# Kernel optimization log

Hardware: AMD Instinct MI355X
Metric: run time of the kernel (lower is better)

## Reference

```python
import jax, jax.numpy as jnp
import numpy as np

B, N, D, H, CD = 2, 2048, 1024, 16, 3
HD = D // H


def setup_inputs() -> dict:
    key = jax.random.key(0)
    ks = jax.random.split(key, 6)
    x = jax.random.normal(ks[0], (B, N, D), dtype=jnp.float32)
    coords = jax.random.normal(ks[1], (B, N, CD), dtype=jnp.float32)
    attn_bias = jax.random.normal(ks[2], (N, N), dtype=jnp.float32) * 0.1
    Wqkv = jax.random.normal(ks[3], (D, 3 * D), dtype=jnp.float32) * (1.0 / np.sqrt(D))
    bqkv = jnp.zeros((3 * D,), dtype=jnp.float32)
    rel_weight = jax.random.normal(ks[4], (H, CD), dtype=jnp.float32) * 0.02
    return {"x": x, "coords": coords, "attn_bias": attn_bias, "Wqkv": Wqkv,
            "bqkv": bqkv, "rel_weight": rel_weight}


def reference(x, coords, attn_bias, Wqkv, bqkv, rel_weight):
    b, n, d = x.shape
    h, hd = H, HD
    qkv = x @ Wqkv + bqkv                       # (B,N,3D)
    q, k, v = jnp.split(qkv, 3, axis=-1)
    # reshape_for_mha: (B,N,D) -> (B,H,N,hd)
    def heads(t):
        return t.reshape(b, n, h, hd).transpose(0, 2, 1, 3)
    qh, kh, vh = heads(q), heads(k), heads(v)
    # coord_proj[b,h,n] = coords[b,n,:] @ rel_weight[h,:]
    coord_proj = jnp.einsum('bnc,hc->bhn', coords.astype(jnp.float32), rel_weight)
    # flex_attention: scale by 1/sqrt(head_dim) BEFORE score_mod
    scores = jnp.einsum('bhqd,bhkd->bhqk', qh, kh) / np.sqrt(hd)
    scores = scores + coord_proj[:, :, :, None] - coord_proj[:, :, None, :]
    scores = scores + attn_bias[None, None, :, :]   # '2d' additive mask bias
    attn = jax.nn.softmax(scores, axis=-1)
    yh = jnp.einsum('bhqk,bhkd->bhqd', attn, vh)    # (B,H,N,hd)
    return yh.transpose(0, 2, 1, 3).reshape(b, n, d)
```

## Files before the change

kernel.cpp:

```cpp
#include <hip/hip_runtime.h>
#include <hip/hip_bf16.h>
#include <math.h>

typedef __hip_bfloat16 bf16;
typedef __bf16  bf16x8 __attribute__((ext_vector_type(8)));
typedef float   f32x4  __attribute__((ext_vector_type(4)));

#define BB 2
#define NN 2048
#define DD 1024
#define HH 16
#define HD 64
#define LOG2E   1.44269504f
#define SCALE_Q 0.18033688f

__device__ __forceinline__ void glds16(const bf16* g, bf16* l) {
    __builtin_amdgcn_global_load_lds((const __attribute__((address_space(1))) void*)g,
                                     (__attribute__((address_space(3))) void*)l, 16, 0, 0);
}
__device__ __forceinline__ unsigned short bfu(float x) {
    bf16 b = __float2bfloat16(x);
    return __builtin_bit_cast(unsigned short, b);
}

__global__ __launch_bounds__(256) void prep(const float* __restrict__ x,
                                            const float* __restrict__ bias,
                                            const float* __restrict__ W,
                                            const float* __restrict__ coords,
                                            const float* __restrict__ relw,
                                            bf16* __restrict__ xb,
                                            float* __restrict__ pbf,
                                            bf16* __restrict__ Wt,
                                            bf16* __restrict__ cpn) {
    __shared__ bf16 tsm[64][65];
    const int bid = blockIdx.x, tid = threadIdx.x;
    if (bid < 2048) {
        size_t i = ((size_t)bid * 256 + tid) * 8;
        float4 a = *(const float4*)(x + i);
        float4 b = *(const float4*)(x + i + 4);
        bf16 t[8];
        t[0] = __float2bfloat16(a.x); t[1] = __float2bfloat16(a.y);
        t[2] = __float2bfloat16(a.z); t[3] = __float2bfloat16(a.w);
        t[4] = __float2bfloat16(b.x); t[5] = __float2bfloat16(b.y);
        t[6] = __float2bfloat16(b.z); t[7] = __float2bfloat16(b.w);
        *(int4*)(xb + i) = *(int4*)t;
    } else if (bid < 2560) {
        int t    = (bid - 2048) * 256 + tid;
        int lane = t & 63;
        int wave = (t >> 6) & 3;
        int kt   = (t >> 8) & 31;
        int Qb   = t >> 13;
        int quad = lane >> 4, l15 = lane & 15;
        float v[32];
#pragma unroll
        for (int j = 0; j < 32; ++j) {
            int qb = j >> 4, g = (j >> 2) & 3, r = j & 3;
            int q = Qb * 128 + wave * 32 + qb * 16 + quad * 4 + r;
            int k = kt * 64 + g * 16 + l15;
            v[j] = LOG2E * bias[(size_t)q * NN + k];
        }
        int4* dst = (int4*)(pbf + (size_t)t * 32);
#pragma unroll
        for (int i = 0; i < 8; ++i) dst[i] = ((int4*)v)[i];
    } else if (bid < 3328) {
        int idx = bid - 2560;
        int n0 = (idx % 48) * 64;
        int k0 = (idx / 48) * 64;
        int tx = tid & 63, tg = tid >> 6;
#pragma unroll
        for (int i = 0; i < 16; ++i) {
            int r = tg + i * 4;
            tsm[r][tx] = __float2bfloat16(W[(size_t)(k0 + r) * 3072 + n0 + tx]);
        }
        __syncthreads();
#pragma unroll
        for (int i = 0; i < 16; ++i) {
            int r = tg + i * 4;
            Wt[(size_t)(n0 + r) * 1024 + k0 + tx] = tsm[tx][r];
        }
    } else {
        int idx = (bid - 3328) * 256 + tid;
        int n  = idx & (NN - 1);
        int bh = idx >> 11;
        int h  = bh & (HH - 1);
        int b  = bh >> 4;
        float acc = 0.f;
#pragma unroll
        for (int c = 0; c < 3; ++c)
            acc += coords[(size_t)(b * NN + n) * 3 + c] * relw[h * 3 + c];
        cpn[idx] = __float2bfloat16(-LOG2E * acc);
    }
}

__global__ __launch_bounds__(256) void qkv_gemm(const bf16* __restrict__ X,
                                                const bf16* __restrict__ W,
                                                const float* __restrict__ bq,
                                                bf16* __restrict__ qo,
                                                bf16* __restrict__ ko,
                                                bf16* __restrict__ vo) {
    __shared__ __align__(16) bf16 As[128 * 32];
    __shared__ __align__(16) bf16 Bs[128 * 32];
    const int tid  = threadIdx.x;
    const int n0   = blockIdx.x * 128;
    const int m0   = blockIdx.y * 128;
    const int wave = tid >> 6, lane = tid & 63, l15 = lane & 15, quad = lane >> 4;
    const int wm   = wave >> 1, wn = wave & 1;

    f32x4 acc[4][4];
    const f32x4 z4 = {0.f, 0.f, 0.f, 0.f};
#pragma unroll
    for (int i = 0; i < 4; ++i)
#pragma unroll
        for (int j = 0; j < 4; ++j) acc[i][j] = z4;

    for (int kt = 0; kt < 1024; kt += 32) {
        __syncthreads();
#pragma unroll
        for (int j = 0; j < 2; ++j) {
            int s   = (wave * 2 + j) * 64 + lane;
            int row = s >> 2;
            int c   = (s & 3) ^ ((row >> 1) & 3);
            glds16(X + (size_t)(m0 + row) * 1024 + kt + c * 8, As + (wave * 2 + j) * 512);
            glds16(W + (size_t)(n0 + row) * 1024 + kt + c * 8, Bs + (wave * 2 + j) * 512);
        }
        __syncthreads();

        bf16x8 a[4], b[4];
#pragma unroll
        for (int mt = 0; mt < 4; ++mt) {
            int ra = wm * 64 + mt * 16 + l15;
            a[mt] = *(const bf16x8*)&As[ra * 32 + ((quad ^ ((ra >> 1) & 3)) * 8)];
        }
#pragma unroll
        for (int nt = 0; nt < 4; ++nt) {
            int rb = wn * 64 + nt * 16 + l15;
            b[nt] = *(const bf16x8*)&Bs[rb * 32 + ((quad ^ ((rb >> 1) & 3)) * 8)];
        }
#pragma unroll
        for (int mt = 0; mt < 4; ++mt)
#pragma unroll
            for (int nt = 0; nt < 4; ++nt)
                acc[mt][nt] = __builtin_amdgcn_mfma_f32_16x16x32_bf16(a[mt], b[nt], acc[mt][nt], 0, 0, 0);
    }

#pragma unroll
    for (int nt = 0; nt < 4; ++nt) {
        int c    = n0 + wn * 64 + nt * 16 + l15;
        int tsel = c >> 10;
        int rem  = c & 1023;
        int h    = rem >> 6, d = rem & 63;
        float bias = bq[c];
        float qs   = (tsel == 0) ? SCALE_Q : 1.0f;
        bf16* outp = (tsel == 0) ? qo : ((tsel == 1) ? ko : vo);
#pragma unroll
        for (int mt = 0; mt < 4; ++mt)
#pragma unroll
            for (int r = 0; r < 4; ++r) {
                int m = m0 + wm * 64 + mt * 16 + quad * 4 + r;
                int b = m >> 11, n = m & (NN - 1);
                outp[((size_t)(b * HH + h) * NN + n) * HD + d] =
                    __float2bfloat16((acc[mt][nt][r] + bias) * qs);
            }
    }
}

__global__ __launch_bounds__(256) void transpose_v(const bf16* __restrict__ vw,
                                                   bf16* __restrict__ vt) {
    __shared__ bf16 t[64][65];
    const int bh = blockIdx.y;
    const int n0 = blockIdx.x * 64;
    const size_t base = (size_t)bh * NN * HD;
    const int tx = threadIdx.x & 63, tg = threadIdx.x >> 6;
#pragma unroll
    for (int i = 0; i < 16; ++i) {
        int r = tg + i * 4;
        t[r][tx] = vw[base + (size_t)(n0 + r) * HD + tx];
    }
    __syncthreads();
#pragma unroll
    for (int i = 0; i < 16; ++i) {
        int d = tg + i * 4;
        vt[base + (size_t)d * NN + n0 + tx] = t[tx][d];
    }
}

__global__ __launch_bounds__(256, 3) void attn(const bf16* __restrict__ Q,
                                               const bf16* __restrict__ K,
                                               const bf16* __restrict__ Vt_g,
                                               const bf16* __restrict__ cpn_g,
                                               const float* __restrict__ pbf,
                                               float* __restrict__ out) {
    __shared__ __align__(16) bf16 Ks[2][64 * 64];
    __shared__ __align__(16) bf16 Vs[2][64 * 64];
    __shared__ __align__(16) unsigned PsW[4][16 * 36];
    __shared__ __align__(16) bf16 cpl[NN];
    const int tid  = threadIdx.x;
    const int Qb   = blockIdx.x;
    const int bh   = blockIdx.y;
    const int b    = bh >> 4, h = bh & 15;
    const int q0   = Qb * 128;
    const int wave = tid >> 6, lane = tid & 63, l15 = lane & 15, quad = lane >> 4;
    const size_t base = (size_t)bh * NN * HD;

    glds16(cpn_g + bh * NN + (wave * 64 + lane) * 8, cpl + wave * 512);

    bf16x8 qf0[2], qf1[2];
#pragma unroll
    for (int qb = 0; qb < 2; ++qb) {
        int qrow = q0 + wave * 32 + qb * 16 + l15;
        qf0[qb] = *(const bf16x8*)&Q[base + (size_t)qrow * HD + quad * 8];
        qf1[qb] = *(const bf16x8*)&Q[base + (size_t)qrow * HD + 32 + quad * 8];
    }

#pragma unroll
    for (int j = 0; j < 2; ++j) {
        int ss  = (wave * 2 + j) * 64 + lane;
        int row = ss >> 3;
        int c   = (ss & 7) ^ (row & 7);
        glds16(K    + base + (size_t)row * HD + c * 8,  Ks[0] + (wave * 2 + j) * 512);
        glds16(Vt_g + base + (size_t)row * NN + c * 8,  Vs[0] + (wave * 2 + j) * 512);
    }

    const f32x4 z4 = {0.f, 0.f, 0.f, 0.f};
    float l_loc[2][4];
    f32x4 o[2][4];
#pragma unroll
    for (int qb = 0; qb < 2; ++qb) {
#pragma unroll
        for (int r = 0; r < 4; ++r) l_loc[qb][r] = 0.f;
#pragma unroll
        for (int t = 0; t < 4; ++t) o[qb][t] = z4;
    }

    for (int t = 0; t < 32; ++t) {
        const int cur = t & 1;
        __syncthreads();
        if (t < 31) {
            int kk1 = (t + 1) * 64;
#pragma unroll
            for (int j = 0; j < 2; ++j) {
                int ss  = (wave * 2 + j) * 64 + lane;
                int row = ss >> 3;
                int c   = (ss & 7) ^ (row & 7);
                glds16(K    + base + (size_t)(kk1 + row) * HD + c * 8, Ks[cur ^ 1] + (wave * 2 + j) * 512);
                glds16(Vt_g + base + (size_t)row * NN + kk1 + c * 8,   Vs[cur ^ 1] + (wave * 2 + j) * 512);
            }
        }

        bf16x8 k0[4], k1[4];
#pragma unroll
        for (int g = 0; g < 4; ++g) {
            int krow = g * 16 + l15, sw = krow & 7;
            k0[g] = *(const bf16x8*)&Ks[cur][krow * 64 + ((quad ^ sw) * 8)];
            k1[g] = *(const bf16x8*)&Ks[cur][krow * 64 + (((4 + quad) ^ sw) * 8)];
        }

        f32x4 s[2][4];
#pragma unroll
        for (int qb = 0; qb < 2; ++qb)
#pragma unroll
            for (int g = 0; g < 4; ++g) {
                s[qb][g] = __builtin_amdgcn_mfma_f32_16x16x32_bf16(qf0[qb], k0[g], z4, 0, 0, 0);
                s[qb][g] = __builtin_amdgcn_mfma_f32_16x16x32_bf16(qf1[qb], k1[g], s[qb][g], 0, 0, 0);
            }

        float mg[4];
#pragma unroll
        for (int g = 0; g < 4; ++g)
            mg[g] = __bfloat162float(cpl[t * 64 + g * 16 + l15]);

        bf16x8 v0[4], v1[4];
#pragma unroll
        for (int tt = 0; tt < 4; ++tt) {
            int drow = tt * 16 + l15, sw = drow & 7;
            v0[tt] = *(const bf16x8*)&Vs[cur][drow * 64 + ((quad ^ sw) * 8)];
            v1[tt] = *(const bf16x8*)&Vs[cur][drow * 64 + (((4 + quad) ^ sw) * 8)];
        }

        const float* bsrc = pbf + ((((size_t)Qb * 32 + t) * 4 + wave) * 64 + lane) * 32;

#pragma unroll
        for (int qb = 0; qb < 2; ++qb) {
            float4 bv[4];
#pragma unroll
            for (int i = 0; i < 4; ++i) bv[i] = ((const float4*)(bsrc + qb * 16))[i];
            const float* bf = (const float*)bv;

            float p[4][4];
#pragma unroll
            for (int g = 0; g < 4; ++g)
#pragma unroll
                for (int r = 0; r < 4; ++r) {
                    float e = __builtin_amdgcn_exp2f(s[qb][g][r] + bf[g * 4 + r] + mg[g]);
                    p[g][r] = e;
                    l_loc[qb][r] += e;
                }
#pragma unroll
            for (int g2 = 0; g2 < 2; ++g2)
#pragma unroll
                for (int r = 0; r < 4; ++r) {
                    unsigned pk = (unsigned)bfu(p[g2][r]) | ((unsigned)bfu(p[g2 + 2][r]) << 16);
                    PsW[wave][(quad * 4 + r) * 36 + g2 * 16 + l15] = pk;
                }
            asm volatile("s_waitcnt lgkmcnt(0)" ::: "memory");
            const int4* pr = (const int4*)&PsW[wave][l15 * 36 + quad * 8];
            int4 da = pr[0], db = pr[1];
            union { unsigned u[4]; bf16x8 v; } u0, u1;
            u0.u[0] = __builtin_amdgcn_perm(da.y, da.x, 0x05040100u);
            u0.u[1] = __builtin_amdgcn_perm(da.w, da.z, 0x05040100u);
            u0.u[2] = __builtin_amdgcn_perm(db.y, db.x, 0x05040100u);
            u0.u[3] = __builtin_amdgcn_perm(db.w, db.z, 0x05040100u);
            u1.u[0] = __builtin_amdgcn_perm(da.y, da.x, 0x07060302u);
            u1.u[1] = __builtin_amdgcn_perm(da.w, da.z, 0x07060302u);
            u1.u[2] = __builtin_amdgcn_perm(db.y, db.x, 0x07060302u);
            u1.u[3] = __builtin_amdgcn_perm(db.w, db.z, 0x07060302u);
#pragma unroll
            for (int tt = 0; tt < 4; ++tt) {
                o[qb][tt] = __builtin_amdgcn_mfma_f32_16x16x32_bf16(u0.v, v0[tt], o[qb][tt], 0, 0, 0);
                o[qb][tt] = __builtin_amdgcn_mfma_f32_16x16x32_bf16(u1.v, v1[tt], o[qb][tt], 0, 0, 0);
            }
        }
    }

#pragma unroll
    for (int qb = 0; qb < 2; ++qb)
#pragma unroll
        for (int r = 0; r < 4; ++r) {
#pragma unroll
            for (int d = 1; d < 16; d <<= 1)
                l_loc[qb][r] += __shfl_xor(l_loc[qb][r], d, 64);
            float inv = 1.0f / l_loc[qb][r];
            int qq = q0 + wave * 32 + qb * 16 + quad * 4 + r;
#pragma unroll
            for (int tt = 0; tt < 4; ++tt)
                out[((size_t)(b * NN + qq)) * DD + h * HD + tt * 16 + l15] =
                    o[qb][tt][r] * inv;
        }
}

extern "C" void kernel_launch(void* const* d_in, const int* in_sizes, int n_in,
                              void* d_out, int out_size, void* d_ws, size_t ws_size,
                              hipStream_t stream) {
    const float* x      = (const float*)d_in[0];
    const float* coords = (const float*)d_in[1];
    const float* abias  = (const float*)d_in[2];
    const float* Wqkv   = (const float*)d_in[3];
    const float* bqkv   = (const float*)d_in[4];
    const float* relw   = (const float*)d_in[5];
    float* out = (float*)d_out;

    char* ws = (char*)d_ws;
    bf16*  xb  = (bf16*)(ws);
    bf16*  vt  = (bf16*)(ws);
    bf16*  qw  = (bf16*)(ws + 8388608);
    bf16*  kw  = (bf16*)(ws + 16777216);
    bf16*  vw  = (bf16*)(ws + 25165824);
    bf16*  Wt  = (bf16*)(ws + 33554432);
    float* pbf = (float*)(ws + 39845888);
    bf16*  cpb = (bf16*)(ws + 56623104);

    prep       <<<dim3(3584),   256, 0, stream>>>(x, abias, Wqkv, coords, relw,
                                                  xb, pbf, Wt, cpb);
    qkv_gemm   <<<dim3(24, 32), 256, 0, stream>>>(xb, Wt, bqkv, qw, kw, vw);
    transpose_v<<<dim3(32, 32), 256, 0, stream>>>(vw, vt);
    attn       <<<dim3(16, 32), 256, 0, stream>>>(qw, kw, vt, cpb, pbf, out);
}
```

Baseline: 233.9 us.

## Use 8-wave attention blocks and write V transposed directly from QKV GEMM

The attention kernel now runs 512 threads per block, with each wave handling 16 query rows instead of 32. This lowers per-wave register use and raises occupancy, and the prep kernel's precomputed bias layout is rearranged to match. The separate transpose_v kernel is dropped, and the QKV GEMM epilogue writes V straight into the head-dim-major layout. That saves a launch and a round trip through memory, at the cost of strided, uncoalesced scalar stores for V.

```diff
diff --git a/kernel.cpp b/kernel.cpp
--- a/kernel.cpp
+++ b/kernel.cpp
@@ -44,26 +44,26 @@
         t[4] = __float2bfloat16(b.x); t[5] = __float2bfloat16(b.y);
         t[6] = __float2bfloat16(b.z); t[7] = __float2bfloat16(b.w);
         *(int4*)(xb + i) = *(int4*)t;
-    } else if (bid < 2560) {
+    } else if (bid < 3072) {
         int t    = (bid - 2048) * 256 + tid;
         int lane = t & 63;
-        int wave = (t >> 6) & 3;
-        int kt   = (t >> 8) & 31;
-        int Qb   = t >> 13;
+        int wave = (t >> 6) & 7;
+        int kt   = (t >> 9) & 31;
+        int Qb   = t >> 14;
         int quad = lane >> 4, l15 = lane & 15;
-        float v[32];
-#pragma unroll
-        for (int j = 0; j < 32; ++j) {
-            int qb = j >> 4, g = (j >> 2) & 3, r = j & 3;
-            int q = Qb * 128 + wave * 32 + qb * 16 + quad * 4 + r;
+        float v[16];
+#pragma unroll
+        for (int j = 0; j < 16; ++j) {
+            int g = j >> 2, r = j & 3;
+            int q = Qb * 128 + wave * 16 + quad * 4 + r;
             int k = kt * 64 + g * 16 + l15;
             v[j] = LOG2E * bias[(size_t)q * NN + k];
         }
-        int4* dst = (int4*)(pbf + (size_t)t * 32);
-#pragma unroll
-        for (int i = 0; i < 8; ++i) dst[i] = ((int4*)v)[i];
-    } else if (bid < 3328) {
-        int idx = bid - 2560;
+        int4* dst = (int4*)(pbf + (size_t)t * 16);
+#pragma unroll
+        for (int i = 0; i < 4; ++i) dst[i] = ((int4*)v)[i];
+    } else if (bid < 3840) {
+        int idx = bid - 3072;
         int n0 = (idx % 48) * 64;
         int k0 = (idx / 48) * 64;
         int tx = tid & 63, tg = tid >> 6;
@@ -79,7 +79,7 @@
             Wt[(size_t)(n0 + r) * 1024 + k0 + tx] = tsm[tx][r];
         }
     } else {
-        int idx = (bid - 3328) * 256 + tid;
+        int idx = (bid - 3840) * 256 + tid;
         int n  = idx & (NN - 1);
         int bh = idx >> 11;
         int h  = bh & (HH - 1);
@@ -97,7 +97,7 @@
                                                 const float* __restrict__ bq,
                                                 bf16* __restrict__ qo,
                                                 bf16* __restrict__ ko,
-                                                bf16* __restrict__ vo) {
+                                                bf16* __restrict__ vt) {
     __shared__ __align__(16) bf16 As[128 * 32];
     __shared__ __align__(16) bf16 Bs[128 * 32];
     const int tid  = threadIdx.x;
@@ -151,40 +151,22 @@
         int h    = rem >> 6, d = rem & 63;
         float bias = bq[c];
         float qs   = (tsel == 0) ? SCALE_Q : 1.0f;
-        bf16* outp = (tsel == 0) ? qo : ((tsel == 1) ? ko : vo);
 #pragma unroll
         for (int mt = 0; mt < 4; ++mt)
 #pragma unroll
             for (int r = 0; r < 4; ++r) {
                 int m = m0 + wm * 64 + mt * 16 + quad * 4 + r;
                 int b = m >> 11, n = m & (NN - 1);
-                outp[((size_t)(b * HH + h) * NN + n) * HD + d] =
-                    __float2bfloat16((acc[mt][nt][r] + bias) * qs);
+                bf16 val = __float2bfloat16((acc[mt][nt][r] + bias) * qs);
+                if (tsel == 2)
+                    vt[((size_t)(b * HH + h) * HD + d) * NN + n] = val;
+                else
+                    ((tsel == 1) ? ko : qo)[((size_t)(b * HH + h) * NN + n) * HD + d] = val;
             }
     }
 }
 
-__global__ __launch_bounds__(256) void transpose_v(const bf16* __restrict__ vw,
-                                                   bf16* __restrict__ vt) {
-    __shared__ bf16 t[64][65];
-    const int bh = blockIdx.y;
-    const int n0 = blockIdx.x * 64;
-    const size_t base = (size_t)bh * NN * HD;
-    const int tx = threadIdx.x & 63, tg = threadIdx.x >> 6;
-#pragma unroll
-    for (int i = 0; i < 16; ++i) {
-        int r = tg + i * 4;
-        t[r][tx] = vw[base + (size_t)(n0 + r) * HD + tx];
-    }
-    __syncthreads();
-#pragma unroll
-    for (int i = 0; i < 16; ++i) {
-        int d = tg + i * 4;
-        vt[base + (size_t)d * NN + n0 + tx] = t[tx][d];
-    }
-}
-
-__global__ __launch_bounds__(256, 3) void attn(const bf16* __restrict__ Q,
+__global__ __launch_bounds__(512, 4) void attn(const bf16* __restrict__ Q,
                                                const bf16* __restrict__ K,
                                                const bf16* __restrict__ Vt_g,
                                                const bf16* __restrict__ cpn_g,
@@ -192,7 +174,7 @@
                                                float* __restrict__ out) {
     __shared__ __align__(16) bf16 Ks[2][64 * 64];
     __shared__ __align__(16) bf16 Vs[2][64 * 64];
-    __shared__ __align__(16) unsigned PsW[4][16 * 36];
+    __shared__ __align__(16) unsigned PsW[8][16 * 36];
     __shared__ __align__(16) bf16 cpl[NN];
     const int tid  = threadIdx.x;
     const int Qb   = blockIdx.x;
@@ -202,140 +184,113 @@
     const int wave = tid >> 6, lane = tid & 63, l15 = lane & 15, quad = lane >> 4;
     const size_t base = (size_t)bh * NN * HD;
 
-    glds16(cpn_g + bh * NN + (wave * 64 + lane) * 8, cpl + wave * 512);
-
-    bf16x8 qf0[2], qf1[2];
-#pragma unroll
-    for (int qb = 0; qb < 2; ++qb) {
-        int qrow = q0 + wave * 32 + qb * 16 + l15;
-        qf0[qb] = *(const bf16x8*)&Q[base + (size_t)qrow * HD + quad * 8];
-        qf1[qb] = *(const bf16x8*)&Q[base + (size_t)qrow * HD + 32 + quad * 8];
-    }
-
-#pragma unroll
-    for (int j = 0; j < 2; ++j) {
-        int ss  = (wave * 2 + j) * 64 + lane;
-        int row = ss >> 3;
-        int c   = (ss & 7) ^ (row & 7);
-        glds16(K    + base + (size_t)row * HD + c * 8,  Ks[0] + (wave * 2 + j) * 512);
-        glds16(Vt_g + base + (size_t)row * NN + c * 8,  Vs[0] + (wave * 2 + j) * 512);
+    if (wave < 4)
+        glds16(cpn_g + bh * NN + (wave * 64 + lane) * 8, cpl + wave * 512);
+
+    const int qrow = q0 + wave * 16 + l15;
+    bf16x8 qf0 = *(const bf16x8*)&Q[base + (size_t)qrow * HD + quad * 8];
+    bf16x8 qf1 = *(const bf16x8*)&Q[base + (size_t)qrow * HD + 32 + quad * 8];
+
+    {
+        int s   = wave * 64 + lane;
+        int row = s >> 3;
+        int c   = (s & 7) ^ (row & 7);
+        glds16(K    + base + (size_t)row * HD + c * 8, Ks[0] + wave * 512);
+        glds16(Vt_g + base + (size_t)row * NN + c * 8, Vs[0] + wave * 512);
     }
 
     const f32x4 z4 = {0.f, 0.f, 0.f, 0.f};
-    float l_loc[2][4];
-    f32x4 o[2][4];
-#pragma unroll
-    for (int qb = 0; qb < 2; ++qb) {
-#pragma unroll
-        for (int r = 0; r < 4; ++r) l_loc[qb][r] = 0.f;
-#pragma unroll
-        for (int t = 0; t < 4; ++t) o[qb][t] = z4;
-    }
+    float l_loc[4] = {0.f, 0.f, 0.f, 0.f};
+    f32x4 o[4];
+#pragma unroll
+    for (int t = 0; t < 4; ++t) o[t] = z4;
 
     for (int t = 0; t < 32; ++t) {
         const int cur = t & 1;
         __syncthreads();
         if (t < 31) {
             int kk1 = (t + 1) * 64;
-#pragma unroll
-            for (int j = 0; j < 2; ++j) {
-                int ss  = (wave * 2 + j) * 64 + lane;
-                int row = ss >> 3;
-                int c   = (ss & 7) ^ (row & 7);
-                glds16(K    + base + (size_t)(kk1 + row) * HD + c * 8, Ks[cur ^ 1] + (wave * 2 + j) * 512);
-                glds16(Vt_g + base + (size_t)row * NN + kk1 + c * 8,   Vs[cur ^ 1] + (wave * 2 + j) * 512);
-            }
-        }
-
-        bf16x8 k0[4], k1[4];
+            int s   = wave * 64 + lane;
+            int row = s >> 3;
+            int c   = (s & 7) ^ (row & 7);
+            glds16(K    + base + (size_t)(kk1 + row) * HD + c * 8, Ks[cur ^ 1] + wave * 512);
+            glds16(Vt_g + base + (size_t)row * NN + kk1 + c * 8,   Vs[cur ^ 1] + wave * 512);
+        }
+
+        f32x4 s4[4];
 #pragma unroll
         for (int g = 0; g < 4; ++g) {
             int krow = g * 16 + l15, sw = krow & 7;
-            k0[g] = *(const bf16x8*)&Ks[cur][krow * 64 + ((quad ^ sw) * 8)];
-            k1[g] = *(const bf16x8*)&Ks[cur][krow * 64 + (((4 + quad) ^ sw) * 8)];
-        }
-
-        f32x4 s[2][4];
-#pragma unroll
-        for (int qb = 0; qb < 2; ++qb)
-#pragma unroll
-            for (int g = 0; g < 4; ++g) {
-                s[qb][g] = __builtin_amdgcn_mfma_f32_16x16x32_bf16(qf0[qb], k0[g], z4, 0, 0, 0);
-                s[qb][g] = __builtin_amdgcn_mfma_f32_16x16x32_bf16(qf1[qb], k1[g], s[qb][g], 0, 0, 0);
-            }
-
+            bf16x8 k0 = *(const bf16x8*)&Ks[cur][krow * 64 + ((quad ^ sw) * 8)];
+            bf16x8 k1 = *(const bf16x8*)&Ks[cur][krow * 64 + (((4 + quad) ^ sw) * 8)];
+            s4[g] = __builtin_amdgcn_mfma_f32_16x16x32_bf16(qf0, k0, z4, 0, 0, 0);
+            s4[g] = __builtin_amdgcn_mfma_f32_16x16x32_bf16(qf1, k1, s4[g], 0, 0, 0);
+        }
+
+        float4 bv[4];
+        {
+            const float* bsrc = pbf + ((((size_t)Qb * 32 + t) * 8 + wave) * 64 + lane) * 16;
+#pragma unroll
+            for (int i = 0; i < 4; ++i) bv[i] = ((const float4*)bsrc)[i];
+        }
+        const float* bf = (const float*)bv;
         float mg[4];
 #pragma unroll
         for (int g = 0; g < 4; ++g)
             mg[g] = __bfloat162float(cpl[t * 64 + g * 16 + l15]);
 
-        bf16x8 v0[4], v1[4];
+        float p[4][4];
+#pragma unroll
+        for (int g = 0; g < 4; ++g)
+#pragma unroll
+            for (int r = 0; r < 4; ++r) {
+                float e = __builtin_amdgcn_exp2f(s4[g][r] + bf[g * 4 + r] + mg[g]);
+                p[g][r] = e;
+                l_loc[r] += e;
+            }
+
+#pragma unroll
+        for (int g2 = 0; g2 < 2; ++g2)
+#pragma unroll
+            for (int r = 0; r < 4; ++r) {
+                unsigned pk = (unsigned)bfu(p[g2][r]) | ((unsigned)bfu(p[g2 + 2][r]) << 16);
+                PsW[wave][(quad * 4 + r) * 36 + g2 * 16 + l15] = pk;
+            }
+        asm volatile("s_waitcnt lgkmcnt(0)" ::: "memory");
+        const int4* pr = (const int4*)&PsW[wave][l15 * 36 + quad * 8];
+        int4 da = pr[0], db = pr[1];
+        union { unsigned u[4]; bf16x8 v; } u0, u1;
+        u0.u[0] = __builtin_amdgcn_perm(da.y, da.x, 0x05040100u);
+        u0.u[1] = __builtin_amdgcn_perm(da.w, da.z, 0x05040100u);
+        u0.u[2] = __builtin_amdgcn_perm(db.y, db.x, 0x05040100u);
+        u0.u[3] = __builtin_amdgcn_perm(db.w, db.z, 0x05040100u);
+        u1.u[0] = __builtin_amdgcn_perm(da.y, da.x, 0x07060302u);
+        u1.u[1] = __builtin_amdgcn_perm(da.w, da.z, 0x07060302u);
+        u1.u[2] = __builtin_amdgcn_perm(db.y, db.x, 0x07060302u);
+        u1.u[3] = __builtin_amdgcn_perm(db.w, db.z, 0x07060302u);
+
 #pragma unroll
         for (int tt = 0; tt < 4; ++tt) {
             int drow = tt * 16 + l15, sw = drow & 7;
-            v0[tt] = *(const bf16x8*)&Vs[cur][drow * 64 + ((quad ^ sw) * 8)];
-            v1[tt] = *(const bf16x8*)&Vs[cur][drow * 64 + (((4 + quad) ^ sw) * 8)];
-        }
-
-        const float* bsrc = pbf + ((((size_t)Qb * 32 + t) * 4 + wave) * 64 + lane) * 32;
-
-#pragma unroll
-        for (int qb = 0; qb < 2; ++qb) {
-            float4 bv[4];
-#pragma unroll
-            for (int i = 0; i < 4; ++i) bv[i] = ((const float4*)(bsrc + qb * 16))[i];
-            const float* bf = (const float*)bv;
-
-            float p[4][4];
-#pragma unroll
-            for (int g = 0; g < 4; ++g)
-#pragma unroll
-                for (int r = 0; r < 4; ++r) {
-                    float e = __builtin_amdgcn_exp2f(s[qb][g][r] + bf[g * 4 + r] + mg[g]);
-                    p[g][r] = e;
-                    l_loc[qb][r] += e;
-                }
-#pragma unroll
-            for (int g2 = 0; g2 < 2; ++g2)
-#pragma unroll
-                for (int r = 0; r < 4; ++r) {
-                    unsigned pk = (unsigned)bfu(p[g2][r]) | ((unsigned)bfu(p[g2 + 2][r]) << 16);
-                    PsW[wave][(quad * 4 + r) * 36 + g2 * 16 + l15] = pk;
-                }
-            asm volatile("s_waitcnt lgkmcnt(0)" ::: "memory");
-            const int4* pr = (const int4*)&PsW[wave][l15 * 36 + quad * 8];
-            int4 da = pr[0], db = pr[1];
-            union { unsigned u[4]; bf16x8 v; } u0, u1;
-            u0.u[0] = __builtin_amdgcn_perm(da.y, da.x, 0x05040100u);
-            u0.u[1] = __builtin_amdgcn_perm(da.w, da.z, 0x05040100u);
-            u0.u[2] = __builtin_amdgcn_perm(db.y, db.x, 0x05040100u);
-            u0.u[3] = __builtin_amdgcn_perm(db.w, db.z, 0x05040100u);
-            u1.u[0] = __builtin_amdgcn_perm(da.y, da.x, 0x07060302u);
-            u1.u[1] = __builtin_amdgcn_perm(da.w, da.z, 0x07060302u);
-            u1.u[2] = __builtin_amdgcn_perm(db.y, db.x, 0x07060302u);
-            u1.u[3] = __builtin_amdgcn_perm(db.w, db.z, 0x07060302u);
-#pragma unroll
-            for (int tt = 0; tt < 4; ++tt) {
-                o[qb][tt] = __builtin_amdgcn_mfma_f32_16x16x32_bf16(u0.v, v0[tt], o[qb][tt], 0, 0, 0);
-                o[qb][tt] = __builtin_amdgcn_mfma_f32_16x16x32_bf16(u1.v, v1[tt], o[qb][tt], 0, 0, 0);
-            }
-        }
-    }
-
-#pragma unroll
-    for (int qb = 0; qb < 2; ++qb)
-#pragma unroll
-        for (int r = 0; r < 4; ++r) {
-#pragma unroll
-            for (int d = 1; d < 16; d <<= 1)
-                l_loc[qb][r] += __shfl_xor(l_loc[qb][r], d, 64);
-            float inv = 1.0f / l_loc[qb][r];
-            int qq = q0 + wave * 32 + qb * 16 + quad * 4 + r;
-#pragma unroll
-            for (int tt = 0; tt < 4; ++tt)
-                out[((size_t)(b * NN + qq)) * DD + h * HD + tt * 16 + l15] =
-                    o[qb][tt][r] * inv;
-        }
+            bf16x8 v0 = *(const bf16x8*)&Vs[cur][drow * 64 + ((quad ^ sw) * 8)];
+            bf16x8 v1 = *(const bf16x8*)&Vs[cur][drow * 64 + (((4 + quad) ^ sw) * 8)];
+            o[tt] = __builtin_amdgcn_mfma_f32_16x16x32_bf16(u0.v, v0, o[tt], 0, 0, 0);
+            o[tt] = __builtin_amdgcn_mfma_f32_16x16x32_bf16(u1.v, v1, o[tt], 0, 0, 0);
+        }
+    }
+
+#pragma unroll
+    for (int r = 0; r < 4; ++r) {
+#pragma unroll
+        for (int d = 1; d < 16; d <<= 1)
+            l_loc[r] += __shfl_xor(l_loc[r], d, 64);
+        float inv = 1.0f / l_loc[r];
+        int qq = q0 + wave * 16 + quad * 4 + r;
+#pragma unroll
+        for (int tt = 0; tt < 4; ++tt)
+            out[((size_t)(b * NN + qq)) * DD + h * HD + tt * 16 + l15] =
+                o[tt][r] * inv;
+    }
 }
 
 extern "C" void kernel_launch(void* const* d_in, const int* in_sizes, int n_in,
@@ -351,17 +306,15 @@
 
     char* ws = (char*)d_ws;
     bf16*  xb  = (bf16*)(ws);
-    bf16*  vt  = (bf16*)(ws);
     bf16*  qw  = (bf16*)(ws + 8388608);
     bf16*  kw  = (bf16*)(ws + 16777216);
-    bf16*  vw  = (bf16*)(ws + 25165824);
+    bf16*  vt  = (bf16*)(ws + 25165824);
     bf16*  Wt  = (bf16*)(ws + 33554432);
     float* pbf = (float*)(ws + 39845888);
     bf16*  cpb = (bf16*)(ws + 56623104);
 
-    prep       <<<dim3(3584),   256, 0, stream>>>(x, abias, Wqkv, coords, relw,
-                                                  xb, pbf, Wt, cpb);
-    qkv_gemm   <<<dim3(24, 32), 256, 0, stream>>>(xb, Wt, bqkv, qw, kw, vw);
-    transpose_v<<<dim3(32, 32), 256, 0, stream>>>(vw, vt);
-    attn       <<<dim3(16, 32), 256, 0, stream>>>(qw, kw, vt, cpb, pbf, out);
-}
+    prep    <<<dim3(4096),   256, 0, stream>>>(x, abias, Wqkv, coords, relw,
+                                               xb, pbf, Wt, cpb);
+    qkv_gemm<<<dim3(24, 32), 256, 0, stream>>>(xb, Wt, bqkv, qw, kw, vt);
+    attn    <<<dim3(16, 32), 512, 0, stream>>>(qw, kw, vt, cpb, pbf, out);
+}
```

Result: faster. 208.6 us (-10.8%).
